# Kernel optimization log

Measured on AMD Instinct MI355X. Metric: run time of the kernel, lower is better.

The kernel has to match this reference:

```python
import jax, jax.numpy as jnp
import numpy as np

NEG_SLOPE = 0.2
EPS = 1e-16  # matches PyG softmax epsilon


def gat_conv(x, src, dst, W, att_src, att_dst, bias):
    """PyG-style GATConv (concat heads, self-loops already in src/dst).
    x: [N, F_in]; W: [F_in, H*C]; att_*: [H, C]; bias: [H*C]."""
    N = x.shape[0]
    H, C = att_src.shape
    h = (x @ W).reshape(N, H, C)                       # [N,H,C]
    a_src = jnp.einsum('nhc,hc->nh', h, att_src)       # [N,H]
    a_dst = jnp.einsum('nhc,hc->nh', h, att_dst)
    e = jax.nn.leaky_relu(a_src[src] + a_dst[dst], NEG_SLOPE)   # [E,H]
    # segment softmax over incoming edges of each dst node
    e_max = jax.ops.segment_max(e, dst, num_segments=N)         # [N,H]
    e_max = jnp.where(jnp.isfinite(e_max), e_max, 0.0)
    e_exp = jnp.exp(e - e_max[dst])                              # [E,H]
    denom = jax.ops.segment_sum(e_exp, dst, num_segments=N)     # [N,H]
    alpha = e_exp / (denom[dst] + EPS)                           # [E,H]
    msg = h[src] * alpha[:, :, None]                             # [E,H,C]
    out = jax.ops.segment_sum(msg, dst, num_segments=N)         # [N,H,C]
    return out.reshape(N, H * C) + bias


def setup_inputs() -> dict:
    key = jax.random.key(0)
    ks = jax.random.split(key, 16)
    N, E = 50000, 800000
    F_in, C, H = 1280, 32, 8
    HC = H * C
    NG = 64  # graphs in batch
    x = jax.random.normal(ks[0], (N, F_in), dtype=jnp.float32)
    edge_index = jax.random.randint(ks[1], (2, E), 0, N, dtype=jnp.int64)
    batch = jnp.sort(jax.random.randint(ks[2], (N,), 0, NG, dtype=jnp.int64))
    s = 1.0 / np.sqrt(F_in)
    W1 = jax.random.normal(ks[3], (F_in, HC), dtype=jnp.float32) * s
    as1 = jax.random.normal(ks[4], (H, C), dtype=jnp.float32) * 0.1
    ad1 = jax.random.normal(ks[5], (H, C), dtype=jnp.float32) * 0.1
    b1 = jnp.zeros((HC,), dtype=jnp.float32)
    s2 = 1.0 / np.sqrt(HC)
    W2 = jax.random.normal(ks[6], (HC, HC), dtype=jnp.float32) * s2
    as2 = jax.random.normal(ks[7], (H, C), dtype=jnp.float32) * 0.1
    ad2 = jax.random.normal(ks[8], (H, C), dtype=jnp.float32) * 0.1
    b2 = jnp.zeros((HC,), dtype=jnp.float32)
    lin1_w = jax.random.normal(ks[9], (HC, 128), dtype=jnp.float32) * s2
    lin1_b = jnp.zeros((128,), dtype=jnp.float32)
    lin2_w = jax.random.normal(ks[10], (128, 1), dtype=jnp.float32) * (1.0 / np.sqrt(128))
    lin2_b = jnp.zeros((1,), dtype=jnp.float32)
    return {"x": x, "edge_index": edge_index, "batch": batch,
            "W1": W1, "as1": as1, "ad1": ad1, "b1": b1,
            "W2": W2, "as2": as2, "ad2": ad2, "b2": b2,
            "lin1_w": lin1_w, "lin1_b": lin1_b, "lin2_w": lin2_w, "lin2_b": lin2_b}


def reference(x, edge_index, batch, W1, as1, ad1, b1, W2, as2, ad2, b2,
              lin1_w, lin1_b, lin2_w, lin2_b):
    N = x.shape[0]
    NG = 64
    loops = jnp.arange(N, dtype=edge_index.dtype)
    src = jnp.concatenate([edge_index[0], loops])  # add self-loops (PyG default)
    dst = jnp.concatenate([edge_index[1], loops])
    h = jax.nn.relu(gat_conv(x, src, dst, W1, as1, ad1, b1))
    h = jax.nn.relu(gat_conv(h, src, dst, W2, as2, ad2, b2))
    # global mean pool over graphs
    sums = jax.ops.segment_sum(h, batch, num_segments=NG)               # [NG,HC]
    cnts = jax.ops.segment_sum(jnp.ones((N, 1), h.dtype), batch, num_segments=NG)
    pooled = sums / jnp.maximum(cnts, 1.0)
    z = jax.nn.relu(pooled @ lin1_w + lin1_b)
    out = z @ lin2_w + lin2_b                                            # [NG,1]
    return out.squeeze(-1)
```

## Files before the change

### kernel.cpp

```cpp
#include <hip/hip_runtime.h>
#include <hip/hip_bf16.h>
#include <math.h>

#define HC 256
#define NH 8
#define NEG_SLOPE 0.2f
#define CHW 64

typedef unsigned short u16;
typedef __attribute__((ext_vector_type(8))) short bf16x8;
typedef __attribute__((ext_vector_type(4))) short bf16x4;
typedef __attribute__((ext_vector_type(4))) float f32x4;

__device__ __forceinline__ u16 f2bf(float f) {
    unsigned int u = __float_as_uint(f);
    u += 0x7FFFu + ((u >> 16) & 1u);
    return (u16)(u >> 16);
}
__device__ __forceinline__ float bf2f(u16 s) {
    return __uint_as_float(((unsigned int)s) << 16);
}
__device__ __forceinline__ f32x4 bf4f(ushort4 v) {
    f32x4 r;
    r[0] = bf2f(v.x); r[1] = bf2f(v.y); r[2] = bf2f(v.z); r[3] = bf2f(v.w);
    return r;
}

#define BAR_LDS()                                                  \
    do {                                                           \
        asm volatile("s_waitcnt lgkmcnt(0)" ::: "memory");         \
        __builtin_amdgcn_s_barrier();                              \
        __builtin_amdgcn_sched_barrier(0);                         \
    } while (0)

__global__ __launch_bounds__(256) void pack_b_split(const float* __restrict__ B, int K,
                                                    u16* __restrict__ Bh,
                                                    u16* __restrict__ Bl) {
    const int g = blockIdx.x * 256 + threadIdx.x;
    const int lane = g & 63;
    const int f = (g >> 6) & 15;
    const int kt = g >> 10;
    const int col = f * 16 + (lane & 15);
    const int k0 = kt * 32 + (lane >> 4) * 8;
    bf16x8 hv, lv;
#pragma unroll
    for (int e = 0; e < 8; e++) {
        const float v = B[(size_t)(k0 + e) * HC + col];
        const u16 h = f2bf(v);
        hv[e] = (short)h;
        lv[e] = (short)f2bf(v - bf2f(h));
    }
    const size_t off = (size_t)g * 8;
    *(bf16x8*)(Bh + off) = hv;
    *(bf16x8*)(Bl + off) = lv;
}

__global__ __launch_bounds__(256) void gemm_fused_split(
    const float* __restrict__ A,
    const u16* __restrict__ Bh, const u16* __restrict__ Bl,
    float* __restrict__ C, int M, int K) {
    __shared__ u16 ldsA[2][64 * 40];
    const int tid = threadIdx.x;
    const int wid = tid >> 6;
    const int lane = tid & 63;
    const int rowblk = blockIdx.x;
    const int KT = K >> 5;

    f32x4 acc[4][4];
#pragma unroll
    for (int i = 0; i < 4; i++)
#pragma unroll
        for (int j = 0; j < 4; j++) acc[i][j] = (f32x4)0.f;

    const int srow = tid >> 2;
    const int sc0 = (tid & 3) * 8;
    const int grow = rowblk * 64 + srow;
    const float* aptr = (grow < M) ? (A + (size_t)grow * K + sc0) : nullptr;
    const int woff = srow * 40 + sc0;

    auto stage = [&](int buf, float4 v0, float4 v1) {
        const float vv[8] = {v0.x, v0.y, v0.z, v0.w, v1.x, v1.y, v1.z, v1.w};
        bf16x8 hv;
#pragma unroll
        for (int e = 0; e < 8; e++) hv[e] = (short)f2bf(vv[e]);
        *(bf16x8*)&ldsA[buf][woff] = hv;
    };
    auto readA = [&](int buf, bf16x8* ah) {
#pragma unroll
        for (int i = 0; i < 4; i++)
            ah[i] = *(const bf16x8*)&ldsA[buf][(i * 16 + (lane & 15)) * 40 +
                                              (lane >> 4) * 8];
    };
    auto loadB = [&](int kt, bf16x8* bh, bf16x8* bl) {
        const u16* bHp = Bh + ((size_t)kt * 16 + wid * 4) * 512 + lane * 8;
        const u16* bLp = Bl + ((size_t)kt * 16 + wid * 4) * 512 + lane * 8;
#pragma unroll
        for (int j = 0; j < 4; j++) {
            bh[j] = *(const bf16x8*)(bHp + j * 512);
            bl[j] = *(const bf16x8*)(bLp + j * 512);
        }
    };
    auto mfma_tile = [&](const bf16x8* ah, const bf16x8* bh, const bf16x8* bl) {
#pragma unroll
        for (int i = 0; i < 4; i++)
#pragma unroll
            for (int j = 0; j < 4; j++) {
                acc[i][j] = __builtin_amdgcn_mfma_f32_16x16x32_bf16(ah[i], bh[j], acc[i][j], 0, 0, 0);
                acc[i][j] = __builtin_amdgcn_mfma_f32_16x16x32_bf16(ah[i], bl[j], acc[i][j], 0, 0, 0);
            }
    };

    float4 a0 = make_float4(0.f, 0.f, 0.f, 0.f), a1 = a0;
    if (aptr) {
        a0 = *(const float4*)(aptr);
        a1 = *(const float4*)(aptr + 4);
    }
    stage(0, a0, a1);
    a0 = make_float4(0.f, 0.f, 0.f, 0.f); a1 = a0;
    if (aptr && KT > 1) {
        a0 = *(const float4*)(aptr + 32);
        a1 = *(const float4*)(aptr + 36);
    }
    BAR_LDS();

    bf16x8 b0h[4], b0l[4], b1h[4], b1l[4];
    loadB(0, b0h, b0l);

    int cur = 0;
    for (int kt = 0; kt < KT; kt += 2) {
        if (kt + 1 < KT) loadB(kt + 1, b1h, b1l);
        bf16x8 ah[4];
        readA(cur, ah);
        stage(cur ^ 1, a0, a1);
        a0 = make_float4(0.f, 0.f, 0.f, 0.f); a1 = a0;
        if (aptr && kt + 2 < KT) {
            a0 = *(const float4*)(aptr + (kt + 2) * 32);
            a1 = *(const float4*)(aptr + (kt + 2) * 32 + 4);
        }
        mfma_tile(ah, b0h, b0l);
        BAR_LDS();
        cur ^= 1;

        if (kt + 2 < KT) loadB(kt + 2, b0h, b0l);
        readA(cur, ah);
        if (kt + 2 < KT) {
            stage(cur ^ 1, a0, a1);
            a0 = make_float4(0.f, 0.f, 0.f, 0.f); a1 = a0;
            if (aptr && kt + 3 < KT) {
                a0 = *(const float4*)(aptr + (kt + 3) * 32);
                a1 = *(const float4*)(aptr + (kt + 3) * 32 + 4);
            }
        }
        mfma_tile(ah, b1h, b1l);
        BAR_LDS();
        cur ^= 1;
    }

    const int r0 = rowblk * 64;
    const int colb = wid * 64 + (lane & 15);
#pragma unroll
    for (int i = 0; i < 4; i++) {
#pragma unroll
        for (int r = 0; r < 4; r++) {
            const int row = r0 + i * 16 + (lane >> 4) * 4 + r;
            if (row < M) {
#pragma unroll
                for (int j = 0; j < 4; j++)
                    C[(size_t)row * HC + colb + j * 16] = acc[i][j][r];
            }
        }
    }
}

__global__ __launch_bounds__(256) void attn_coef(const float* __restrict__ h,
                                                 const float* __restrict__ att_s,
                                                 const float* __restrict__ att_d,
                                                 float* __restrict__ a_src,
                                                 float* __restrict__ a_dst,
                                                 u16* __restrict__ h_bf) {
    const int n = blockIdx.x;
    const int tid = threadIdx.x;
    const float hv = h[(size_t)n * HC + tid];
    h_bf[(size_t)n * HC + tid] = f2bf(hv);
    float p = hv * att_s[tid];
    float q = hv * att_d[tid];
#pragma unroll
    for (int m = 16; m >= 1; m >>= 1) {
        p += __shfl_xor(p, m);
        q += __shfl_xor(q, m);
    }
    if ((tid & 31) == 0) {
        a_src[n * NH + (tid >> 5)] = p;
        a_dst[n * NH + (tid >> 5)] = q;
    }
}

__global__ void count_deg(const int* __restrict__ dst, int E, int ET, int* __restrict__ deg) {
    const int e = blockIdx.x * blockDim.x + threadIdx.x;
    if (e >= ET) return;
    const int d = (e < E) ? dst[e] : (e - E);
    atomicAdd(&deg[d], 1);
}

__global__ __launch_bounds__(256) void scan_block(const int* __restrict__ deg,
                                                  int* __restrict__ row_ptr,
                                                  int* __restrict__ partials, int N) {
    __shared__ int sd[256];
    const int tid = threadIdx.x;
    const int base = blockIdx.x * 1024 + tid * 4;
    int v0 = (base + 0 < N) ? deg[base + 0] : 0;
    int v1 = (base + 1 < N) ? deg[base + 1] : 0;
    int v2 = (base + 2 < N) ? deg[base + 2] : 0;
    int v3 = (base + 3 < N) ? deg[base + 3] : 0;
    const int tsum = v0 + v1 + v2 + v3;
    sd[tid] = tsum;
    __syncthreads();
    int run = tsum;
    for (int off = 1; off < 256; off <<= 1) {
        int t = 0;
        if (tid >= off) t = sd[tid - off];
        __syncthreads();
        run += t;
        sd[tid] = run;
        __syncthreads();
    }
    const int excl = run - tsum;
    int s0 = excl + v0, s1 = s0 + v1, s2 = s1 + v2, s3 = s2 + v3;
    if (base + 0 < N) row_ptr[base + 1] = s0;
    if (base + 1 < N) row_ptr[base + 2] = s1;
    if (base + 2 < N) row_ptr[base + 3] = s2;
    if (base + 3 < N) row_ptr[base + 4] = s3;
    if (tid == 255) partials[blockIdx.x] = run;
}

__global__ __launch_bounds__(1024) void scan_partials(int* __restrict__ partials, int nb) {
    __shared__ int sd[1024];
    const int tid = threadIdx.x;
    int v = (tid < nb) ? partials[tid] : 0;
    sd[tid] = v;
    __syncthreads();
    int run = v;
    for (int off = 1; off < 1024; off <<= 1) {
        int t = 0;
        if (tid >= off) t = sd[tid - off];
        __syncthreads();
        run += t;
        sd[tid] = run;
        __syncthreads();
    }
    if (tid < nb) partials[tid] = run - v;
}

__global__ __launch_bounds__(256) void scan_add(int* __restrict__ row_ptr,
                                                const int* __restrict__ partials, int N) {
    const int i = blockIdx.x * 256 + threadIdx.x;
    if (i == 0) row_ptr[0] = 0;
    if (i < N) row_ptr[i + 1] += partials[i >> 10];
}

__global__ void scatter_edges(const int* __restrict__ src_in, const int* __restrict__ dst,
                              int E, int ET, const int* __restrict__ row_ptr,
                              int* __restrict__ cursor, int* __restrict__ esrc) {
    const int e = blockIdx.x * blockDim.x + threadIdx.x;
    if (e >= ET) return;
    const int d = (e < E) ? dst[e] : (e - E);
    const int s = (e < E) ? src_in[e] : (e - E);
    const int pos = atomicAdd(&cursor[d], 1);
    esrc[row_ptr[d] + pos] = s;
}

__global__ __launch_bounds__(256) void gat_aggregate_wave(
    const u16* __restrict__ h_bf, const float* __restrict__ a_src,
    const float* __restrict__ a_dst, const int* __restrict__ row_ptr,
    const int* __restrict__ esrc, const float* __restrict__ bias,
    float* __restrict__ out, int N) {
    __shared__ int   s_src[4][CHW];
    __shared__ float s_ev[4][CHW][NH];

    const int tid = threadIdx.x;
    const int wv = tid >> 6;
    const int lane = tid & 63;
    const int n = blockIdx.x * 4 + wv;
    if (n >= N) return;

    const int beg = row_ptr[n];
    const int deg = row_ptr[n + 1] - beg;
    const int jj = lane >> 3;
    const int hh = lane & 7;
    const int g4 = lane >> 3;

    const float adh = a_dst[n * NH + hh];
    float m_run = -1e30f, d_run = 0.f;
    f32x4 acc = (f32x4)0.f;

    for (int c0 = 0; c0 < deg; c0 += CHW) {
        const int chlen = min(CHW, deg - c0);

        float lmax = -1e30f;
        for (int p = 0; p < chlen; p += 8) {
            const int j = p + jj;
            if (j < chlen) {
                const int s = esrc[beg + c0 + j];
                if (hh == 0) s_src[wv][j] = s;
                float v = a_src[s * NH + hh] + adh;
                v = (v > 0.f) ? v : NEG_SLOPE * v;
                s_ev[wv][j][hh] = v;
                lmax = fmaxf(lmax, v);
            }
        }
        lmax = fmaxf(lmax, __shfl_xor(lmax, 8));
        lmax = fmaxf(lmax, __shfl_xor(lmax, 16));
        lmax = fmaxf(lmax, __shfl_xor(lmax, 32));
        const float mo = m_run;
        const float mn = fmaxf(mo, lmax);
        const float scl = __expf(mo - mn);
        m_run = mn;

        float lsum = 0.f;
        for (int p = 0; p < chlen; p += 8) {
            const int j = p + jj;
            if (j < chlen) {
                const float pv = __expf(s_ev[wv][j][hh] - mn);
                s_ev[wv][j][hh] = pv;
                lsum += pv;
            }
        }
        lsum += __shfl_xor(lsum, 8);
        lsum += __shfl_xor(lsum, 16);
        lsum += __shfl_xor(lsum, 32);
        d_run = d_run * scl + lsum;

        __asm__ volatile("s_waitcnt lgkmcnt(0)" ::: "memory");

        const float scl4 = __shfl(scl, g4);
        f32x4 t0 = (f32x4)0.f, t1 = (f32x4)0.f, t2 = (f32x4)0.f, t3 = (f32x4)0.f;
        int j = 0;
        for (; j + 4 <= chlen; j += 4) {
            const int s0 = s_src[wv][j],     s1 = s_src[wv][j + 1];
            const int s2 = s_src[wv][j + 2], s3 = s_src[wv][j + 3];
            const float p0 = s_ev[wv][j][g4],     p1 = s_ev[wv][j + 1][g4];
            const float p2 = s_ev[wv][j + 2][g4], p3 = s_ev[wv][j + 3][g4];
            const f32x4 h0 = bf4f(*(const ushort4*)&h_bf[(size_t)s0 * HC + lane * 4]);
            const f32x4 h1 = bf4f(*(const ushort4*)&h_bf[(size_t)s1 * HC + lane * 4]);
            const f32x4 h2 = bf4f(*(const ushort4*)&h_bf[(size_t)s2 * HC + lane * 4]);
            const f32x4 h3 = bf4f(*(const ushort4*)&h_bf[(size_t)s3 * HC + lane * 4]);
#pragma unroll
            for (int q = 0; q < 4; q++) {
                t0[q] += p0 * h0[q];
                t1[q] += p1 * h1[q];
                t2[q] += p2 * h2[q];
                t3[q] += p3 * h3[q];
            }
        }
        for (; j < chlen; j++) {
            const int s0 = s_src[wv][j];
            const float p0 = s_ev[wv][j][g4];
            const f32x4 h0 = bf4f(*(const ushort4*)&h_bf[(size_t)s0 * HC + lane * 4]);
#pragma unroll
            for (int q = 0; q < 4; q++) t0[q] += p0 * h0[q];
        }
#pragma unroll
        for (int q = 0; q < 4; q++)
            acc[q] = acc[q] * scl4 + ((t0[q] + t1[q]) + (t2[q] + t3[q]));
    }

    const float invd = 1.f / (__shfl(d_run, g4) + 1e-16f);
    const f32x4 bv = *(const f32x4*)&bias[lane * 4];
    f32x4 o;
#pragma unroll
    for (int q = 0; q < 4; q++) o[q] = fmaxf(acc[q] * invd + bv[q], 0.f);
    *(f32x4*)&out[(size_t)n * HC + lane * 4] = o;
}

__global__ __launch_bounds__(256) void pool_partial(const float* __restrict__ h,
                                                    const int* __restrict__ batch, int N,
                                                    float* __restrict__ sums) {
    __shared__ int bs[64];
    const int tid = threadIdx.x;
    const int base = blockIdx.x * 64;
    const int cnt = min(64, N - base);
    if (tid < 64 && tid < cnt) bs[tid] = batch[base + tid];
    __syncthreads();

    float acc = 0.f;
    int cur = bs[0];
    for (int i = 0; i < cnt; i++) {
        const int g = bs[i];
        if (g != cur) {
            atomicAdd(&sums[(size_t)cur * HC + tid], acc);
            acc = 0.f;
            cur = g;
        }
        acc += h[(size_t)(base + i) * HC + tid];
    }
    atomicAdd(&sums[(size_t)cur * HC + tid], acc);
}

__global__ __launch_bounds__(256) void pool_div(float* __restrict__ sums,
                                                const int* __restrict__ batch, int N) {
    const int g = blockIdx.x;
    const int tid = threadIdx.x;
    int lo = 0, hi = N;
    while (lo < hi) {
        const int mid = (lo + hi) >> 1;
        if (batch[mid] < g) lo = mid + 1; else hi = mid;
    }
    const int start = lo;
    hi = N;
    while (lo < hi) {
        const int mid = (lo + hi) >> 1;
        if (batch[mid] < g + 1) lo = mid + 1; else hi = mid;
    }
    const float inv = 1.f / fmaxf((float)(lo - start), 1.0f);
    sums[(size_t)g * HC + tid] *= inv;
}

__global__ __launch_bounds__(128) void mlp_head(const float* __restrict__ pooled,
                                                const float* __restrict__ w1,
                                                const float* __restrict__ b1,
                                                const float* __restrict__ w2,
                                                const float* __restrict__ b2,
                                                float* __restrict__ out) {
    const int g = blockIdx.x;
    const int tid = threadIdx.x;
    __shared__ float p[HC];
    p[tid] = pooled[g * HC + tid];
    p[tid + 128] = pooled[g * HC + tid + 128];
    __syncthreads();
    float z = b1[tid];
#pragma unroll 8
    for (int k = 0; k < HC; k++) z += p[k] * w1[k * 128 + tid];
    z = fmaxf(z, 0.f);
    float t = z * w2[tid];
#pragma unroll
    for (int m = 32; m >= 1; m >>= 1) t += __shfl_xor(t, m);
    __shared__ float ws2[2];
    if ((tid & 63) == 0) ws2[tid >> 6] = t;
    __syncthreads();
    if (tid == 0) out[g] = ws2[0] + ws2[1] + b2[0];
}

extern "C" void kernel_launch(void* const* d_in, const int* in_sizes, int n_in,
                              void* d_out, int out_size, void* d_ws, size_t ws_size,
                              hipStream_t stream) {
    const float* x      = (const float*)d_in[0];
    const int*   ei     = (const int*)d_in[1];
    const int*   batch  = (const int*)d_in[2];
    const float* W1     = (const float*)d_in[3];
    const float* as1    = (const float*)d_in[4];
    const float* ad1    = (const float*)d_in[5];
    const float* b1     = (const float*)d_in[6];
    const float* W2     = (const float*)d_in[7];
    const float* as2    = (const float*)d_in[8];
    const float* ad2    = (const float*)d_in[9];
    const float* b2     = (const float*)d_in[10];
    const float* lin1w  = (const float*)d_in[11];
    const float* lin1b  = (const float*)d_in[12];
    const float* lin2w  = (const float*)d_in[13];
    const float* lin2b  = (const float*)d_in[14];

    const int N   = in_sizes[2];
    const int E   = in_sizes[1] / 2;
    const int ET  = E + N;
    const int Fin = in_sizes[0] / N;
    const int NG  = 64;

    const int nRB = (N + 63) / 64;
    const int nScanBlk = (N + 1023) / 1024;

    const int* src_arr = ei;
    const int* dst_arr = ei + E;

    char* ws = (char*)d_ws;
    size_t off = 0;
    auto alloc = [&](size_t bytes) {
        void* p = ws + off;
        off += (bytes + 255) & ~(size_t)255;
        return p;
    };
    float* h_gemm  = (float*)alloc((size_t)N * HC * sizeof(float));
    float* h_agg   = (float*)alloc((size_t)N * HC * sizeof(float));
    u16*   h_bf    = (u16*)alloc((size_t)N * HC * sizeof(u16));
    float* a_src   = (float*)alloc((size_t)N * NH * sizeof(float));
    float* a_dst   = (float*)alloc((size_t)N * NH * sizeof(float));
    int*   deg     = (int*)alloc((size_t)N * sizeof(int));
    int*   cursor  = (int*)alloc((size_t)N * sizeof(int));
    int*   row_ptr = (int*)alloc((size_t)(N + 1) * sizeof(int));
    int*   partials= (int*)alloc((size_t)1024 * sizeof(int));
    int*   esrc    = (int*)alloc((size_t)ET * sizeof(int));
    float* pooled  = (float*)alloc((size_t)NG * HC * sizeof(float));
    u16* Bh = (u16*)alloc((size_t)Fin * HC * sizeof(u16));
    u16* Bl = (u16*)alloc((size_t)Fin * HC * sizeof(u16));
    (void)ws_size; (void)n_in; (void)out_size;

    hipMemsetAsync(deg, 0, (size_t)N * sizeof(int), stream);
    hipMemsetAsync(cursor, 0, (size_t)N * sizeof(int), stream);
    {
        const int blocks = (ET + 255) / 256;
        count_deg<<<blocks, 256, 0, stream>>>(dst_arr, E, ET, deg);
        scan_block<<<nScanBlk, 256, 0, stream>>>(deg, row_ptr, partials, N);
        scan_partials<<<1, 1024, 0, stream>>>(partials, nScanBlk);
        scan_add<<<(N + 255) / 256, 256, 0, stream>>>(row_ptr, partials, N);
        scatter_edges<<<blocks, 256, 0, stream>>>(src_arr, dst_arr, E, ET, row_ptr,
                                                  cursor, esrc);
    }

    const int aggBlocks = (N + 3) / 4;

    pack_b_split<<<(Fin / 32) * 4, 256, 0, stream>>>(W1, Fin, Bh, Bl);
    gemm_fused_split<<<nRB, 256, 0, stream>>>(x, Bh, Bl, h_gemm, N, Fin);
    attn_coef<<<N, 256, 0, stream>>>(h_gemm, as1, ad1, a_src, a_dst, h_bf);
    gat_aggregate_wave<<<aggBlocks, 256, 0, stream>>>(h_bf, a_src, a_dst, row_ptr,
                                                      esrc, b1, h_agg, N);

    pack_b_split<<<(HC / 32) * 4, 256, 0, stream>>>(W2, HC, Bh, Bl);
    gemm_fused_split<<<nRB, 256, 0, stream>>>(h_agg, Bh, Bl, h_gemm, N, HC);
    attn_coef<<<N, 256, 0, stream>>>(h_gemm, as2, ad2, a_src, a_dst, h_bf);
    gat_aggregate_wave<<<aggBlocks, 256, 0, stream>>>(h_bf, a_src, a_dst, row_ptr,
                                                      esrc, b2, h_agg, N);

    hipMemsetAsync(pooled, 0, (size_t)NG * HC * sizeof(float), stream);
    pool_partial<<<(N + 63) / 64, 256, 0, stream>>>(h_agg, batch, N, pooled);
    pool_div<<<NG, 256, 0, stream>>>(pooled, batch, N);
    mlp_head<<<NG, 128, 0, stream>>>(pooled, lin1w, lin1b, lin2w, lin2b, (float*)d_out);
}
```

Before: 508.3 us.

## Stage A in 128-wide K groups to cut GEMM barriers

After: 524.3 us. 3.2% more time.

```diff
diff --git a/kernel.cpp b/kernel.cpp
--- a/kernel.cpp
+++ b/kernel.cpp
@@ -6,10 +6,10 @@
 #define NH 8
 #define NEG_SLOPE 0.2f
 #define CHW 64
+#define LDA 136
 
 typedef unsigned short u16;
 typedef __attribute__((ext_vector_type(8))) short bf16x8;
-typedef __attribute__((ext_vector_type(4))) short bf16x4;
 typedef __attribute__((ext_vector_type(4))) float f32x4;
 
 __device__ __forceinline__ u16 f2bf(float f) {
@@ -59,12 +59,13 @@
     const float* __restrict__ A,
     const u16* __restrict__ Bh, const u16* __restrict__ Bl,
     float* __restrict__ C, int M, int K) {
-    __shared__ u16 ldsA[2][64 * 40];
+    __shared__ u16 ldsA[2][64 * LDA];
     const int tid = threadIdx.x;
     const int wid = tid >> 6;
     const int lane = tid & 63;
     const int rowblk = blockIdx.x;
     const int KT = K >> 5;
+    const int NG4 = K >> 7;
 
     f32x4 acc[4][4];
 #pragma unroll
@@ -73,23 +74,37 @@
         for (int j = 0; j < 4; j++) acc[i][j] = (f32x4)0.f;
 
     const int srow = tid >> 2;
-    const int sc0 = (tid & 3) * 8;
+    const int scc = (tid & 3) * 32;
     const int grow = rowblk * 64 + srow;
-    const float* aptr = (grow < M) ? (A + (size_t)grow * K + sc0) : nullptr;
-    const int woff = srow * 40 + sc0;
-
-    auto stage = [&](int buf, float4 v0, float4 v1) {
-        const float vv[8] = {v0.x, v0.y, v0.z, v0.w, v1.x, v1.y, v1.z, v1.w};
-        bf16x8 hv;
-#pragma unroll
-        for (int e = 0; e < 8; e++) hv[e] = (short)f2bf(vv[e]);
-        *(bf16x8*)&ldsA[buf][woff] = hv;
+    const float* aptr = (grow < M) ? (A + (size_t)grow * K + scc) : nullptr;
+    const int woff = srow * LDA + scc;
+
+    float4 pf[8];
+    auto loadAg = [&](int g) {
+#pragma unroll
+        for (int q = 0; q < 8; q++) {
+            pf[q] = make_float4(0.f, 0.f, 0.f, 0.f);
+            if (aptr) pf[q] = *(const float4*)(aptr + g * 128 + q * 4);
+        }
     };
-    auto readA = [&](int buf, bf16x8* ah) {
+    auto stageg = [&](int buf) {
+#pragma unroll
+        for (int p = 0; p < 4; p++) {
+            const float vv[8] = {pf[2 * p].x,     pf[2 * p].y,
+                                 pf[2 * p].z,     pf[2 * p].w,
+                                 pf[2 * p + 1].x, pf[2 * p + 1].y,
+                                 pf[2 * p + 1].z, pf[2 * p + 1].w};
+            bf16x8 hv;
+#pragma unroll
+            for (int e = 0; e < 8; e++) hv[e] = (short)f2bf(vv[e]);
+            *(bf16x8*)&ldsA[buf][woff + p * 8] = hv;
+        }
+    };
+    auto readA = [&](int buf, int kk, bf16x8* ah) {
 #pragma unroll
         for (int i = 0; i < 4; i++)
-            ah[i] = *(const bf16x8*)&ldsA[buf][(i * 16 + (lane & 15)) * 40 +
-                                              (lane >> 4) * 8];
+            ah[i] = *(const bf16x8*)&ldsA[buf][(i * 16 + (lane & 15)) * LDA +
+                                              kk * 32 + (lane >> 4) * 8];
     };
     auto loadB = [&](int kt, bf16x8* bh, bf16x8* bl) {
         const u16* bHp = Bh + ((size_t)kt * 16 + wid * 4) * 512 + lane * 8;
@@ -110,48 +125,43 @@
             }
     };
 
-    float4 a0 = make_float4(0.f, 0.f, 0.f, 0.f), a1 = a0;
-    if (aptr) {
-        a0 = *(const float4*)(aptr);
-        a1 = *(const float4*)(aptr + 4);
-    }
-    stage(0, a0, a1);
-    a0 = make_float4(0.f, 0.f, 0.f, 0.f); a1 = a0;
-    if (aptr && KT > 1) {
-        a0 = *(const float4*)(aptr + 32);
-        a1 = *(const float4*)(aptr + 36);
-    }
-    BAR_LDS();
-
+    loadAg(0);
+    stageg(0);
+    if (NG4 > 1) loadAg(1);
     bf16x8 b0h[4], b0l[4], b1h[4], b1l[4];
     loadB(0, b0h, b0l);
+    BAR_LDS();
 
     int cur = 0;
-    for (int kt = 0; kt < KT; kt += 2) {
-        if (kt + 1 < KT) loadB(kt + 1, b1h, b1l);
-        bf16x8 ah[4];
-        readA(cur, ah);
-        stage(cur ^ 1, a0, a1);
-        a0 = make_float4(0.f, 0.f, 0.f, 0.f); a1 = a0;
-        if (aptr && kt + 2 < KT) {
-            a0 = *(const float4*)(aptr + (kt + 2) * 32);
-            a1 = *(const float4*)(aptr + (kt + 2) * 32 + 4);
-        }
-        mfma_tile(ah, b0h, b0l);
-        BAR_LDS();
-        cur ^= 1;
-
-        if (kt + 2 < KT) loadB(kt + 2, b0h, b0l);
-        readA(cur, ah);
-        if (kt + 2 < KT) {
-            stage(cur ^ 1, a0, a1);
-            a0 = make_float4(0.f, 0.f, 0.f, 0.f); a1 = a0;
-            if (aptr && kt + 3 < KT) {
-                a0 = *(const float4*)(aptr + (kt + 3) * 32);
-                a1 = *(const float4*)(aptr + (kt + 3) * 32 + 4);
-            }
-        }
-        mfma_tile(ah, b1h, b1l);
+    for (int g = 0; g < NG4; ++g) {
+        if (g + 1 < NG4) stageg(cur ^ 1);
+        if (g + 2 < NG4) loadAg(g + 2);
+
+        const int kt0 = g * 4;
+        {
+            loadB(kt0 + 1 < KT ? kt0 + 1 : kt0, b1h, b1l);
+            bf16x8 ah[4];
+            readA(cur, 0, ah);
+            mfma_tile(ah, b0h, b0l);
+        }
+        {
+            loadB(kt0 + 2 < KT ? kt0 + 2 : kt0, b0h, b0l);
+            bf16x8 ah[4];
+            readA(cur, 1, ah);
+            mfma_tile(ah, b1h, b1l);
+        }
+        {
+            loadB(kt0 + 3 < KT ? kt0 + 3 : kt0, b1h, b1l);
+            bf16x8 ah[4];
+            readA(cur, 2, ah);
+            mfma_tile(ah, b0h, b0l);
+        }
+        {
+            loadB(kt0 + 4 < KT ? kt0 + 4 : kt0, b0h, b0l);
+            bf16x8 ah[4];
+            readA(cur, 3, ah);
+            mfma_tile(ah, b1h, b1l);
+        }
         BAR_LDS();
         cur ^= 1;
     }
```
